# Performance work log

Hardware: AMD Instinct MI355X
Metric: run time of the kernel (lower is better)

## Reference

```python
import jax, jax.numpy as jnp
import numpy as np

BN_EPS = 1e-5


def setup_inputs() -> dict:
    key = jax.random.key(0)
    ks = jax.random.split(key, 5)
    B, T, N, C, O, K, E = 2, 4, 50000, 32, 32, 3, 800000
    x = jax.random.normal(ks[0], (B, T, N, C), dtype=jnp.float32)
    edge_index = jax.random.randint(ks[1], (2, E), 0, N, dtype=jnp.int64)
    edge_weight = jax.random.uniform(ks[2], (E,), dtype=jnp.float32)
    W = jax.random.normal(ks[3], (K, C, O), dtype=jnp.float32) * 0.05
    bias = jnp.zeros((O,), dtype=jnp.float32)
    gamma = jnp.ones((O,), dtype=jnp.float32)
    beta = jnp.zeros((O,), dtype=jnp.float32)
    return {"x": x, "edge_index": edge_index, "edge_weight": edge_weight,
            "W": W, "bias": bias, "gamma": gamma, "beta": beta}


def reference(x, edge_index, edge_weight, W, bias, gamma, beta):
    # x: [B, T, N, C]; edge_index: [2, E]; W: [K, C, O]
    B, T, N, C = x.shape
    K = W.shape[0]
    src, dst = edge_index[0], edge_index[1]

    # Scaled Laplacian L_hat = 2L/lambda_max - I with sym norm, lambda_max=2
    # => L_hat = -D^{-1/2} A D^{-1/2} (zero diagonal), PyG ChebConv default.
    deg = jax.ops.segment_sum(edge_weight, src, num_segments=N)
    safe = jnp.where(deg > 0, deg, 1.0)
    dinv = jnp.where(deg > 0, 1.0 / jnp.sqrt(safe), 0.0)
    norm = -dinv[src] * edge_weight * dinv[dst]  # [E]

    # Batch all (b, t) slices together: [N, M, C] with M = B*T
    xn = jnp.transpose(x, (2, 0, 1, 3)).reshape(N, B * T, C)

    def lap(z):  # sparse SpMM applied to every (b,t) slice at once
        return jax.ops.segment_sum(norm[:, None, None] * z[src], dst,
                                   num_segments=N)

    # Chebyshev recursion: T0 = x, T1 = L_hat x, Tk = 2 L_hat T_{k-1} - T_{k-2}
    Tx_prev2 = xn
    out = jnp.einsum('nmc,co->nmo', Tx_prev2, W[0])
    if K > 1:
        Tx_prev = lap(xn)
        out = out + jnp.einsum('nmc,co->nmo', Tx_prev, W[1])
        for k in range(2, K):
            Tx_k = 2.0 * lap(Tx_prev) - Tx_prev2
            out = out + jnp.einsum('nmc,co->nmo', Tx_k, W[k])
            Tx_prev2, Tx_prev = Tx_prev, Tx_k
    out = out + bias  # [N, M, O]

    # BatchNorm1d in training mode, applied per (b,t) slice over nodes,
    # exactly as the original per-slice loop does (biased variance).
    mean = jnp.mean(out, axis=0, keepdims=True)              # [1, M, O]
    var = jnp.mean((out - mean) ** 2, axis=0, keepdims=True)  # [1, M, O]
    y = gamma * (out - mean) * jax.lax.rsqrt(var + BN_EPS) + beta
    y = jax.nn.relu(y)

    return jnp.transpose(y.reshape(N, B, T, -1), (1, 2, 0, 3))  # [B,T,N,O]
```

## Files before the change

kernel.cpp:

```cpp
#include <hip/hip_runtime.h>

#define NNODES 50000
#define NEDGES 800000
#define MB 8
#define CF 32
#define OF 32
#define FPN 256
#define TOTAL_OUT (MB * NNODES * OF)

#define BSH 9
#define BINW 512
#define NB ((NNODES + BINW - 1) / BINW)
#define PH (NB * 2)
#define NBA 1024
#define EPB ((NEDGES + NBA - 1) / NBA)
#define CAPL 20
#define LBW 24
#define CH 8
#define BINCAP 13312
#define STCAP 7168
#define WFB ((NNODES / 16 + 3) / 4)

typedef unsigned short ushort_t;
typedef unsigned int uint_t;
typedef __attribute__((ext_vector_type(8))) short bf16x8;
typedef __attribute__((ext_vector_type(4))) float f32x4;

__device__ __forceinline__ ushort_t f2bf(float f) {
    uint_t u = __float_as_uint(f);
    u += 0x7FFFu + ((u >> 16) & 1u);
    return (ushort_t)(u >> 16);
}
__device__ __forceinline__ float bflo(uint_t u) { return __uint_as_float(u << 16); }
__device__ __forceinline__ float bfhi(uint_t u) { return __uint_as_float(u & 0xFFFF0000u); }

__device__ __forceinline__ bool detect_is64(const int* ei) {
    int lane = threadIdx.x & 63;
    int v = ei[2 * lane + 1];
    return __ballot(v != 0) == 0ULL;
}

__global__ void __launch_bounds__(256) k_build(const int* __restrict__ ei,
                                               const float* __restrict__ w,
                                               const float* __restrict__ x,
                                               int* __restrict__ g_cntD,
                                               int* __restrict__ g_cntS,
                                               int* __restrict__ g_realH,
                                               int2* __restrict__ binD,
                                               int2* __restrict__ binS,
                                               ushort_t* __restrict__ xn) {
    int blk = blockIdx.x;
    int t = threadIdx.x;
    __shared__ int l_cnt[NB];
    __shared__ int l_base[NB];
    __shared__ ushort_t l_pfx[NB + 1];
    __shared__ int l_half[PH];
    __shared__ int2 l_buf[NB][LBW];
    if (blk < NBA) {
        bool is64 = detect_is64(ei);
        const int2* ei2 = (const int2*)ei;
        for (int i = t; i < NB; i += 256) l_cnt[i] = 0;
        for (int i = t; i < PH; i += 256) l_half[i] = 0;
        __syncthreads();
        int e0 = blk * EPB;
        int e1 = min(e0 + EPB, NEDGES);
        int sreg[4];
        float wreg[4];
        #pragma unroll
        for (int i = 0; i < 4; i++) {
            int e = e0 + t + i * 256;
            bool ok = (e < e1);
            int s = 0, d = 0;
            float wt = 0.0f;
            if (ok) {
                if (is64) {
                    s = ei2[e].x;
                    d = ei2[NEDGES + e].x;
                } else {
                    s = ei[e];
                    d = ei[NEDGES + e];
                }
                wt = w[e];
            }
            sreg[i] = ok ? s : -1;
            wreg[i] = wt;
            if (ok) {
                int bin = d >> BSH;
                int half = (d >> 8) & 1;
                int2 entry;
                entry.x = s | ((d & (BINW - 1)) << 16);
                entry.y = __float_as_int(wt);
                int pos = atomicAdd(&l_cnt[bin], 1);
                if (pos < CAPL) {
                    l_buf[bin][pos] = entry;
                    atomicAdd(&l_half[bin * 2 + half], 1);
                } else {
                    int gp = atomicAdd(&g_cntD[bin], 1);
                    if (gp < BINCAP) {
                        binD[(size_t)bin * BINCAP + gp] = entry;
                        atomicAdd(&g_realH[bin * 2 + half], 1);
                    }
                }
            }
        }
        __syncthreads();
        if (t < NB) {
            int c = min(l_cnt[t], CAPL);
            int p = (c + CH - 1) & ~(CH - 1);
            for (int i = c; i < p; i++) l_buf[t][i] = make_int2(0, 0);
            l_cnt[t] = p;
            if (p > 0) l_base[t] = atomicAdd(&g_cntD[t], p);
        }
        for (int i = t; i < PH; i += 256)
            if (l_half[i] > 0) atomicAdd(&g_realH[i], l_half[i]);
        __syncthreads();
        if (t == 0) {
            int sacc = 0;
            for (int b2 = 0; b2 < NB; b2++) {
                l_pfx[b2] = (ushort_t)sacc;
                sacc += l_cnt[b2];
            }
            l_pfx[NB] = (ushort_t)sacc;
        }
        __syncthreads();
        {
            int total = l_pfx[NB];
            for (int idx = t; idx < total; idx += 256) {
                int lo = 0, hi = NB - 1;
                while (lo < hi) {
                    int mid = (lo + hi + 1) >> 1;
                    if ((int)l_pfx[mid] <= idx) lo = mid; else hi = mid - 1;
                }
                int rel = idx - (int)l_pfx[lo];
                int gp = l_base[lo] + rel;
                if (gp < BINCAP) binD[(size_t)lo * BINCAP + gp] = l_buf[lo][rel];
            }
        }
        __syncthreads();
        for (int i = t; i < NB; i += 256) l_cnt[i] = 0;
        __syncthreads();
        #pragma unroll
        for (int i = 0; i < 4; i++) {
            if (sreg[i] >= 0) {
                int s = sreg[i];
                int bin = s >> BSH;
                int2 entry;
                entry.x = s & (BINW - 1);
                entry.y = __float_as_int(wreg[i]);
                int pos = atomicAdd(&l_cnt[bin], 1);
                if (pos < CAPL) {
                    l_buf[bin][pos] = entry;
                } else {
                    int gp = atomicAdd(&g_cntS[bin], 1);
                    if (gp < BINCAP) binS[(size_t)bin * BINCAP + gp] = entry;
                }
            }
        }
        __syncthreads();
        if (t < NB) {
            int c = min(l_cnt[t], CAPL);
            int p = (c + CH - 1) & ~(CH - 1);
            for (int i = c; i < p; i++) l_buf[t][i] = make_int2(0, 0);
            l_cnt[t] = p;
            if (p > 0) l_base[t] = atomicAdd(&g_cntS[t], p);
        }
        __syncthreads();
        if (t == 0) {
            int sacc = 0;
            for (int b2 = 0; b2 < NB; b2++) {
                l_pfx[b2] = (ushort_t)sacc;
                sacc += l_cnt[b2];
            }
            l_pfx[NB] = (ushort_t)sacc;
        }
        __syncthreads();
        {
            int total = l_pfx[NB];
            for (int idx = t; idx < total; idx += 256) {
                int lo = 0, hi = NB - 1;
                while (lo < hi) {
                    int mid = (lo + hi + 1) >> 1;
                    if ((int)l_pfx[mid] <= idx) lo = mid; else hi = mid - 1;
                }
                int rel = idx - (int)l_pfx[lo];
                int gp = l_base[lo] + rel;
                if (gp < BINCAP) binS[(size_t)lo * BINCAP + gp] = l_buf[lo][rel];
            }
        }
    } else {
        int bb = blk - NBA;
        int lane = t & 63;
        int n = bb * 4 + (t >> 6);
        int m = lane >> 3;
        int c = (4 * lane) & 31;
        const float4 v = *(const float4*)(x + ((size_t)m * NNODES + n) * CF + c);
        uint2 d;
        d.x = (uint_t)f2bf(v.x) | ((uint_t)f2bf(v.y) << 16);
        d.y = (uint_t)f2bf(v.z) | ((uint_t)f2bf(v.w) << 16);
        *(uint2*)(xn + (size_t)n * FPN + 4 * lane) = d;
    }
}

__global__ void __launch_bounds__(256) k_deg(const int* __restrict__ g_cntS,
                                             const int2* __restrict__ binS,
                                             float* __restrict__ dinv) {
    __shared__ float l_acc[BINW];
    int b = blockIdx.x;
    int t = threadIdx.x;
    l_acc[t] = 0.0f;
    l_acc[t + 256] = 0.0f;
    __syncthreads();
    int cnt = min(g_cntS[b], BINCAP);
    const int2* bp = binS + (size_t)b * BINCAP;
    for (int i = t; i < cnt; i += 256) {
        int2 e = bp[i];
        atomicAdd(&l_acc[e.x], __int_as_float(e.y));
    }
    __syncthreads();
    #pragma unroll
    for (int i = 0; i < 2; i++) {
        int idx = i * 256 + t;
        int n = b * BINW + idx;
        if (n < NNODES) {
            float s = l_acc[idx];
            dinv[n] = (s > 0.0f) ? (1.0f / sqrtf(s)) : 0.0f;
        }
    }
}

__global__ void __launch_bounds__(256) k_pass2(const int* __restrict__ g_cntD,
                                               const int* __restrict__ g_realH,
                                               const int2* __restrict__ binD,
                                               const float* __restrict__ dinv,
                                               int2* __restrict__ csr,
                                               int* __restrict__ csr_off) {
    __shared__ int2 l_stage[STCAP];
    __shared__ int l_h[256];
    __shared__ int l_ws[4];
    __shared__ int l_red[4];
    __shared__ int l_tot;
    int b = blockIdx.x;
    int t = threadIdx.x;
    int bin = b >> 1, h = b & 1;
    int lane = t & 63, wv = t >> 6;

    int vb = (t < b) ? g_realH[t] : 0;
    #pragma unroll
    for (int off = 32; off >= 1; off >>= 1) vb += __shfl_down(vb, off);
    if (lane == 0) l_red[wv] = vb;
    l_h[t] = 0;
    __syncthreads();
    int base = l_red[0] + l_red[1] + l_red[2] + l_red[3];

    int cnt = min(g_cntD[bin], BINCAP);
    const int2* bp = binD + (size_t)bin * BINCAP;
    for (int i = t; i < cnt; i += 256) {
        int2 e = bp[i];
        int dl = e.x >> 16;
        if (e.y != 0 && (dl >> 8) == h) atomicAdd(&l_h[dl & 255], 1);
    }
    __syncthreads();

    int a0 = l_h[t];
    int v = a0;
    #pragma unroll
    for (int off = 1; off < 64; off <<= 1) {
        int u = __shfl_up(v, off);
        if (lane >= off) v += u;
    }
    if (lane == 63) l_ws[wv] = v;
    __syncthreads();
    int wpre = 0;
    for (int i = 0; i < wv; i++) wpre += l_ws[i];
    int excl = wpre + v - a0;

    int n = bin * BINW + h * 256 + t;
    if (n < NNODES) csr_off[n] = base + excl;
    l_h[t] = excl;
    if (t == 255) {
        l_tot = excl + a0;
        if (b == PH - 1) csr_off[NNODES] = base + excl + a0;
    }
    __syncthreads();

    for (int i = t; i < cnt; i += 256) {
        int2 e = bp[i];
        int dl = e.x >> 16;
        if (e.y != 0 && (dl >> 8) == h) {
            int src = e.x & 0xFFFF;
            int dst = bin * BINW + dl;
            float val = -dinv[src] * __int_as_float(e.y) * dinv[dst];
            int slot = atomicAdd(&l_h[dl & 255], 1);
            if (slot < STCAP) l_stage[slot] = make_int2(src, __float_as_int(val));
        }
    }
    __syncthreads();

    int tot = min(l_tot, STCAP);
    for (int i = t; i < tot; i += 256) csr[(size_t)base + i] = l_stage[i];
}

template <int PHASE>
__global__ void __launch_bounds__(256) k_spmm(const ushort_t* __restrict__ src,
                                              const ushort_t* __restrict__ xn0,
                                              const int* __restrict__ csr_off,
                                              const int2* __restrict__ csr,
                                              ushort_t* __restrict__ dst) {
    int t = threadIdx.x;
    int lane = t & 63;
    int n = __builtin_amdgcn_readfirstlane(blockIdx.x * 4 + (t >> 6));
    int off = csr_off[n];
    int cnt = min(csr_off[n + 1] - off, 64);
    float a0 = 0.0f, a1 = 0.0f, a2 = 0.0f, a3 = 0.0f;
    if (cnt > 0) {
        int j = off + min(lane, cnt - 1);
        int2 ed = csr[j];
        int cv = ed.x;
        uint_t vv = (uint_t)ed.y;
        for (int k = 0; k < cnt; k += 16) {
            int sc[16]; float v[16];
            #pragma unroll
            for (int i = 0; i < 16; i++) {
                sc[i] = __builtin_amdgcn_readlane(cv, k + i);
                float vr = __uint_as_float(__builtin_amdgcn_readlane((int)vv, k + i));
                v[i] = (k + i < cnt) ? vr : 0.0f;
            }
            uint2 u[16];
            #pragma unroll
            for (int i = 0; i < 16; i++)
                u[i] = *(const uint2*)(src + (size_t)sc[i] * FPN + 4 * lane);
            #pragma unroll
            for (int i = 0; i < 16; i++) {
                a0 += v[i] * bflo(u[i].x);
                a1 += v[i] * bfhi(u[i].x);
                a2 += v[i] * bflo(u[i].y);
                a3 += v[i] * bfhi(u[i].y);
            }
        }
    }
    if (PHASE == 2) {
        const uint2 xu = *(const uint2*)(xn0 + (size_t)n * FPN + 4 * lane);
        a0 = 2.0f * a0 - bflo(xu.x);
        a1 = 2.0f * a1 - bfhi(xu.x);
        a2 = 2.0f * a2 - bflo(xu.y);
        a3 = 2.0f * a3 - bfhi(xu.y);
    }
    uint2 d;
    d.x = (uint_t)f2bf(a0) | ((uint_t)f2bf(a1) << 16);
    d.y = (uint_t)f2bf(a2) | ((uint_t)f2bf(a3) << 16);
    *(uint2*)(dst + (size_t)n * FPN + 4 * lane) = d;
}

__global__ void k_wprep(const float* __restrict__ W, ushort_t* __restrict__ wbf) {
    int tid = threadIdx.x;
    for (int i = tid; i < 384; i += 256) {
        int k    = i >> 7;
        int rem  = i & 127;
        int oh   = rem >> 6;
        int lane = rem & 63;
        int quad = lane >> 4;
        int colc = lane & 15;
        ushort_t* d = wbf + (size_t)i * 8;
        for (int j = 0; j < 8; j++) {
            int c = quad * 8 + j;
            int o = oh * 16 + colc;
            d[j] = f2bf(W[k * (CF * OF) + c * OF + o]);
        }
    }
}

__global__ void __launch_bounds__(256) k_wfuse(const ushort_t* __restrict__ xn,
                                               const ushort_t* __restrict__ t1,
                                               const ushort_t* __restrict__ t2,
                                               const ushort_t* __restrict__ wbf,
                                               const float* __restrict__ bias,
                                               float* __restrict__ out) {
    int t = threadIdx.x;
    int lane = t & 63;
    int wv = blockIdx.x * 4 + (t >> 6);
    if (wv >= NNODES / 16) return;
    int n0 = wv * 16;
    int quad = lane >> 4, col = lane & 15;

    bf16x8 B[6];
    #pragma unroll
    for (int i = 0; i < 6; i++)
        B[i] = *(const bf16x8*)(wbf + (size_t)(i * 64 + lane) * 8);
    float blo = bias[col], bhi = bias[16 + col];

    size_t aoff = (size_t)(n0 + col) * FPN + quad * 8;
    #pragma unroll
    for (int m = 0; m < 8; m++) {
        bf16x8 A0 = *(const bf16x8*)(xn + aoff + m * 32);
        bf16x8 A1 = *(const bf16x8*)(t1 + aoff + m * 32);
        bf16x8 A2 = *(const bf16x8*)(t2 + aoff + m * 32);
        f32x4 lo = { blo, blo, blo, blo };
        f32x4 hi = { bhi, bhi, bhi, bhi };
        lo = __builtin_amdgcn_mfma_f32_16x16x32_bf16(A0, B[0], lo, 0, 0, 0);
        hi = __builtin_amdgcn_mfma_f32_16x16x32_bf16(A0, B[1], hi, 0, 0, 0);
        lo = __builtin_amdgcn_mfma_f32_16x16x32_bf16(A1, B[2], lo, 0, 0, 0);
        hi = __builtin_amdgcn_mfma_f32_16x16x32_bf16(A1, B[3], hi, 0, 0, 0);
        lo = __builtin_amdgcn_mfma_f32_16x16x32_bf16(A2, B[4], lo, 0, 0, 0);
        hi = __builtin_amdgcn_mfma_f32_16x16x32_bf16(A2, B[5], hi, 0, 0, 0);
        float* ob = out + ((size_t)m * NNODES + n0 + quad * 4) * OF + col;
        #pragma unroll
        for (int r = 0; r < 4; r++) {
            ob[(size_t)r * OF]      = lo[r];
            ob[(size_t)r * OF + 16] = hi[r];
        }
    }
}

__global__ void __launch_bounds__(256) k_stats(const float* __restrict__ out,
                                               float* __restrict__ stats) {
    int m = blockIdx.y;
    int t = threadIdx.x;
    int o4 = t & 7, row = t >> 3;
    int n0 = blockIdx.x * 1024;
    int nend = min(n0 + 1024, NNODES);
    float sx = 0, sy = 0, sz = 0, sw = 0;
    float qx = 0, qy = 0, qz = 0, qw = 0;
    for (int n = n0 + row; n < nend; n += 32) {
        const float4 v = *(const float4*)(out + ((size_t)m * NNODES + n) * OF + o4 * 4);
        sx += v.x; sy += v.y; sz += v.z; sw += v.w;
        qx += v.x * v.x; qy += v.y * v.y; qz += v.z * v.z; qw += v.w * v.w;
    }
    __shared__ float4 sS[256];
    __shared__ float4 sQ[256];
    sS[t] = make_float4(sx, sy, sz, sw);
    sQ[t] = make_float4(qx, qy, qz, qw);
    __syncthreads();
    for (int off = 16; off >= 1; off >>= 1) {
        if (row < off) {
            float4 a = sS[t], b = sS[t + off * 8];
            sS[t] = make_float4(a.x + b.x, a.y + b.y, a.z + b.z, a.w + b.w);
            float4 c = sQ[t], d = sQ[t + off * 8];
            sQ[t] = make_float4(c.x + d.x, c.y + d.y, c.z + d.z, c.w + d.w);
        }
        __syncthreads();
    }
    if (row == 0) {
        float4 s = sS[t], q = sQ[t];
        int base = m * 32 + o4 * 4;
        atomicAdd(&stats[base + 0], s.x);
        atomicAdd(&stats[base + 1], s.y);
        atomicAdd(&stats[base + 2], s.z);
        atomicAdd(&stats[base + 3], s.w);
        atomicAdd(&stats[256 + base + 0], q.x);
        atomicAdd(&stats[256 + base + 1], q.y);
        atomicAdd(&stats[256 + base + 2], q.z);
        atomicAdd(&stats[256 + base + 3], q.w);
    }
}

__global__ void __launch_bounds__(256) k_final(float* __restrict__ out,
                                               const float* __restrict__ stats,
                                               const float* __restrict__ gamma,
                                               const float* __restrict__ beta) {
    int idx4 = blockIdx.x * 256 + threadIdx.x;
    size_t base = (size_t)idx4 * 4;
    int o = (int)(base & 31);
    int m = (int)(base / ((size_t)NNODES * OF));
    int mo = m * 32 + o;
    const float4 sm = *(const float4*)(stats + mo);
    const float4 sq = *(const float4*)(stats + 256 + mo);
    const float4 g  = *(const float4*)(gamma + o);
    const float4 bt = *(const float4*)(beta + o);
    const float inv_n = 1.0f / (float)NNODES;
    float4 v = *(const float4*)(out + base);
    {
        float mean = sm.x * inv_n, var = sq.x * inv_n - mean * mean;
        float sc = g.x * rsqrtf(var + 1e-5f);
        v.x = fmaxf(v.x * sc + (bt.x - sc * mean), 0.0f);
    }
    {
        float mean = sm.y * inv_n, var = sq.y * inv_n - mean * mean;
        float sc = g.y * rsqrtf(var + 1e-5f);
        v.y = fmaxf(v.y * sc + (bt.y - sc * mean), 0.0f);
    }
    {
        float mean = sm.z * inv_n, var = sq.z * inv_n - mean * mean;
        float sc = g.z * rsqrtf(var + 1e-5f);
        v.z = fmaxf(v.z * sc + (bt.z - sc * mean), 0.0f);
    }
    {
        float mean = sm.w * inv_n, var = sq.w * inv_n - mean * mean;
        float sc = g.w * rsqrtf(var + 1e-5f);
        v.w = fmaxf(v.w * sc + (bt.w - sc * mean), 0.0f);
    }
    *(float4*)(out + base) = v;
}

extern "C" void kernel_launch(void* const* d_in, const int* in_sizes, int n_in,
                              void* d_out, int out_size, void* d_ws, size_t ws_size,
                              hipStream_t stream) {
    const float* x     = (const float*)d_in[0];
    const int*   ei    = (const int*)d_in[1];
    const float* w     = (const float*)d_in[2];
    const float* W     = (const float*)d_in[3];
    const float* bias  = (const float*)d_in[4];
    const float* gamma = (const float*)d_in[5];
    const float* beta  = (const float*)d_in[6];
    float* out = (float*)d_out;

    char* p = (char*)d_ws;
    auto alloc = [&](size_t bytes) {
        char* r = p;
        p += (bytes + 511) & ~(size_t)511;
        return r;
    };
    int*      g_cntD  = (int*)alloc((size_t)NB * 4);
    int*      g_cntS  = (int*)alloc((size_t)NB * 4);
    int*      g_realH = (int*)alloc((size_t)PH * 4);
    float*    stats   = (float*)alloc(512 * 4);
    float*    dinv    = (float*)alloc((size_t)NNODES * 4);
    int2*     binD    = (int2*)alloc((size_t)NB * BINCAP * 8);
    int2*     binS    = (int2*)alloc((size_t)NB * BINCAP * 8);
    int2*     csr     = (int2*)alloc((size_t)NEDGES * 8);
    int*      csr_off = (int*)alloc((size_t)(NNODES + 1) * 4);
    ushort_t* wbf     = (ushort_t*)alloc(384 * 8 * 2);
    ushort_t* xn      = (ushort_t*)alloc((size_t)NNODES * FPN * 2);
    ushort_t* t1      = (ushort_t*)alloc((size_t)NNODES * FPN * 2);
    ushort_t* t2      = (ushort_t*)alloc((size_t)NNODES * FPN * 2);

    size_t zlen = (char*)(stats + 512) - (char*)g_cntD;
    hipMemsetAsync(g_cntD, 0, zlen, stream);

    k_wprep<<<1, 256, 0, stream>>>(W, wbf);
    k_build<<<NBA + NNODES / 4, 256, 0, stream>>>(ei, w, x, g_cntD, g_cntS,
                                                  g_realH, binD, binS, xn);
    k_deg<<<NB, 256, 0, stream>>>(g_cntS, binS, dinv);
    k_pass2<<<PH, 256, 0, stream>>>(g_cntD, g_realH, binD, dinv, csr, csr_off);

    k_spmm<1><<<NNODES / 4, 256, 0, stream>>>(xn, xn, csr_off, csr, t1);
    k_spmm<2><<<NNODES / 4, 256, 0, stream>>>(t1, xn, csr_off, csr, t2);

    k_wfuse<<<WFB, 256, 0, stream>>>(xn, t1, t2, wbf, bias, out);

    dim3 sgrid((NNODES + 1023) / 1024, MB);
    k_stats<<<sgrid, 256, 0, stream>>>(out, stats);
    k_final<<<TOTAL_OUT / 4 / 256, 256, 0, stream>>>(out, stats, gamma, beta);
}
```

Baseline: 366.6 us.

## Fuse degree and CSR build, fold norm into SpMM, fuse second SpMM with MFMA

Merges k_deg and k_pass2 into one launch whose CSR slots sit at a fixed offset per half-bin, each row padded to a multiple of 16 with the padded count packed into csr_off. This drops the global realH prefix counts. The dinv-based normalization moves into the SpMM kernels, and the second SpMM is fused with the weight MFMA through LDS, so the t2 buffer is never written or read. The memset and weight prep fold into one init kernel. In exchange the CSR has fixed capacity with padded zero edges, per-node edges beyond 64 are silently truncated, and dinv is recomputed per edge in both SpMMs.

```diff
diff --git a/kernel.cpp b/kernel.cpp
--- a/kernel.cpp
+++ b/kernel.cpp
@@ -18,8 +18,7 @@
 #define LBW 24
 #define CH 8
 #define BINCAP 13312
-#define STCAP 7168
-#define WFB ((NNODES / 16 + 3) / 4)
+#define STCAP 7936
 
 typedef unsigned short ushort_t;
 typedef unsigned int uint_t;
@@ -38,6 +37,31 @@
     int lane = threadIdx.x & 63;
     int v = ei[2 * lane + 1];
     return __ballot(v != 0) == 0ULL;
+}
+
+__global__ void __launch_bounds__(256) k_init(const float* __restrict__ W,
+                                              ushort_t* __restrict__ wbf,
+                                              int* __restrict__ g_cntD,
+                                              int* __restrict__ g_cntS,
+                                              float* __restrict__ stats) {
+    int t = threadIdx.x;
+    if (t < NB) { g_cntD[t] = 0; g_cntS[t] = 0; }
+    stats[t] = 0.0f;
+    stats[256 + t] = 0.0f;
+    for (int i = t; i < 384; i += 256) {
+        int k    = i >> 7;
+        int rem  = i & 127;
+        int oh   = rem >> 6;
+        int lane = rem & 63;
+        int quad = lane >> 4;
+        int colc = lane & 15;
+        ushort_t* d = wbf + (size_t)i * 8;
+        for (int j = 0; j < 8; j++) {
+            int c = quad * 8 + j;
+            int o = oh * 16 + colc;
+            d[j] = f2bf(W[k * (CF * OF) + c * OF + o]);
+        }
+    }
 }
 
 __global__ void __launch_bounds__(256) k_build(const int* __restrict__ ei,
@@ -45,7 +69,6 @@
                                                const float* __restrict__ x,
                                                int* __restrict__ g_cntD,
                                                int* __restrict__ g_cntS,
-                                               int* __restrict__ g_realH,
                                                int2* __restrict__ binD,
                                                int2* __restrict__ binS,
                                                ushort_t* __restrict__ xn) {
@@ -54,13 +77,11 @@
     __shared__ int l_cnt[NB];
     __shared__ int l_base[NB];
     __shared__ ushort_t l_pfx[NB + 1];
-    __shared__ int l_half[PH];
     __shared__ int2 l_buf[NB][LBW];
     if (blk < NBA) {
         bool is64 = detect_is64(ei);
         const int2* ei2 = (const int2*)ei;
         for (int i = t; i < NB; i += 256) l_cnt[i] = 0;
-        for (int i = t; i < PH; i += 256) l_half[i] = 0;
         __syncthreads();
         int e0 = blk * EPB;
         int e1 = min(e0 + EPB, NEDGES);
@@ -86,20 +107,15 @@
             wreg[i] = wt;
             if (ok) {
                 int bin = d >> BSH;
-                int half = (d >> 8) & 1;
                 int2 entry;
                 entry.x = s | ((d & (BINW - 1)) << 16);
                 entry.y = __float_as_int(wt);
                 int pos = atomicAdd(&l_cnt[bin], 1);
                 if (pos < CAPL) {
                     l_buf[bin][pos] = entry;
-                    atomicAdd(&l_half[bin * 2 + half], 1);
                 } else {
                     int gp = atomicAdd(&g_cntD[bin], 1);
-                    if (gp < BINCAP) {
-                        binD[(size_t)bin * BINCAP + gp] = entry;
-                        atomicAdd(&g_realH[bin * 2 + half], 1);
-                    }
+                    if (gp < BINCAP) binD[(size_t)bin * BINCAP + gp] = entry;
                 }
             }
         }
@@ -111,8 +127,6 @@
             l_cnt[t] = p;
             if (p > 0) l_base[t] = atomicAdd(&g_cntD[t], p);
         }
-        for (int i = t; i < PH; i += 256)
-            if (l_half[i] > 0) atomicAdd(&g_realH[i], l_half[i]);
         __syncthreads();
         if (t == 0) {
             int sacc = 0;
@@ -201,57 +215,48 @@
     }
 }
 
-__global__ void __launch_bounds__(256) k_deg(const int* __restrict__ g_cntS,
-                                             const int2* __restrict__ binS,
-                                             float* __restrict__ dinv) {
-    __shared__ float l_acc[BINW];
+__global__ void __launch_bounds__(256) k_prep(const int* __restrict__ g_cntD,
+                                              const int* __restrict__ g_cntS,
+                                              const int2* __restrict__ binD,
+                                              const int2* __restrict__ binS,
+                                              float* __restrict__ dinv,
+                                              int2* __restrict__ csr,
+                                              int* __restrict__ csr_off) {
+    __shared__ int2 l_stage[STCAP];
+    __shared__ int l_h[256];
+    __shared__ int l_end[256];
+    __shared__ int l_ws[4];
     int b = blockIdx.x;
     int t = threadIdx.x;
-    l_acc[t] = 0.0f;
-    l_acc[t + 256] = 0.0f;
-    __syncthreads();
-    int cnt = min(g_cntS[b], BINCAP);
-    const int2* bp = binS + (size_t)b * BINCAP;
-    for (int i = t; i < cnt; i += 256) {
-        int2 e = bp[i];
-        atomicAdd(&l_acc[e.x], __int_as_float(e.y));
-    }
-    __syncthreads();
-    #pragma unroll
-    for (int i = 0; i < 2; i++) {
-        int idx = i * 256 + t;
-        int n = b * BINW + idx;
-        if (n < NNODES) {
-            float s = l_acc[idx];
-            dinv[n] = (s > 0.0f) ? (1.0f / sqrtf(s)) : 0.0f;
-        }
-    }
-}
-
-__global__ void __launch_bounds__(256) k_pass2(const int* __restrict__ g_cntD,
-                                               const int* __restrict__ g_realH,
-                                               const int2* __restrict__ binD,
-                                               const float* __restrict__ dinv,
-                                               int2* __restrict__ csr,
-                                               int* __restrict__ csr_off) {
-    __shared__ int2 l_stage[STCAP];
-    __shared__ int l_h[256];
-    __shared__ int l_ws[4];
-    __shared__ int l_red[4];
-    __shared__ int l_tot;
-    int b = blockIdx.x;
-    int t = threadIdx.x;
-    int bin = b >> 1, h = b & 1;
+    if (b < NB) {
+        float* l_acc = (float*)l_stage;
+        l_acc[t] = 0.0f;
+        l_acc[t + 256] = 0.0f;
+        __syncthreads();
+        int cnt = min(g_cntS[b], BINCAP);
+        const int2* bp = binS + (size_t)b * BINCAP;
+        for (int i = t; i < cnt; i += 256) {
+            int2 e = bp[i];
+            atomicAdd(&l_acc[e.x], __int_as_float(e.y));
+        }
+        __syncthreads();
+        #pragma unroll
+        for (int i = 0; i < 2; i++) {
+            int idx = i * 256 + t;
+            int n = b * BINW + idx;
+            if (n < NNODES) {
+                float s = l_acc[idx];
+                dinv[n] = (s > 0.0f) ? (1.0f / sqrtf(s)) : 0.0f;
+            }
+        }
+        return;
+    }
+    int b2 = b - NB;
+    int bin = b2 >> 1, h = b2 & 1;
     int lane = t & 63, wv = t >> 6;
 
-    int vb = (t < b) ? g_realH[t] : 0;
-    #pragma unroll
-    for (int off = 32; off >= 1; off >>= 1) vb += __shfl_down(vb, off);
-    if (lane == 0) l_red[wv] = vb;
     l_h[t] = 0;
     __syncthreads();
-    int base = l_red[0] + l_red[1] + l_red[2] + l_red[3];
-
     int cnt = min(g_cntD[bin], BINCAP);
     const int2* bp = binD + (size_t)bin * BINCAP;
     for (int i = t; i < cnt; i += 256) {
@@ -261,8 +266,9 @@
     }
     __syncthreads();
 
-    int a0 = l_h[t];
-    int v = a0;
+    int hreal = l_h[t];
+    int ppad = min((hreal + 15) & ~15, 64);
+    int v = ppad;
     #pragma unroll
     for (int off = 1; off < 64; off <<= 1) {
         int u = __shfl_up(v, off);
@@ -272,63 +278,62 @@
     __syncthreads();
     int wpre = 0;
     for (int i = 0; i < wv; i++) wpre += l_ws[i];
-    int excl = wpre + v - a0;
+    int excl = wpre + v - ppad;
+    int tot = l_ws[0] + l_ws[1] + l_ws[2] + l_ws[3];
+    int ztot = min(tot, STCAP);
 
     int n = bin * BINW + h * 256 + t;
-    if (n < NNODES) csr_off[n] = base + excl;
+    if (n < NNODES) csr_off[n] = ((b2 * STCAP + excl) << 3) | (ppad >> 4);
     l_h[t] = excl;
-    if (t == 255) {
-        l_tot = excl + a0;
-        if (b == PH - 1) csr_off[NNODES] = base + excl + a0;
-    }
-    __syncthreads();
-
+    l_end[t] = min(excl + ppad, STCAP);
+    __syncthreads();
+
+    for (int i = t; i < ztot; i += 256) l_stage[i] = make_int2(0, 0);
+    __syncthreads();
     for (int i = t; i < cnt; i += 256) {
         int2 e = bp[i];
         int dl = e.x >> 16;
         if (e.y != 0 && (dl >> 8) == h) {
-            int src = e.x & 0xFFFF;
-            int dst = bin * BINW + dl;
-            float val = -dinv[src] * __int_as_float(e.y) * dinv[dst];
-            int slot = atomicAdd(&l_h[dl & 255], 1);
-            if (slot < STCAP) l_stage[slot] = make_int2(src, __float_as_int(val));
-        }
-    }
-    __syncthreads();
-
-    int tot = min(l_tot, STCAP);
-    for (int i = t; i < tot; i += 256) csr[(size_t)base + i] = l_stage[i];
-}
-
-template <int PHASE>
-__global__ void __launch_bounds__(256) k_spmm(const ushort_t* __restrict__ src,
-                                              const ushort_t* __restrict__ xn0,
-                                              const int* __restrict__ csr_off,
-                                              const int2* __restrict__ csr,
-                                              ushort_t* __restrict__ dst) {
+            int node = dl & 255;
+            int slot = atomicAdd(&l_h[node], 1);
+            if (slot < l_end[node]) l_stage[slot] = make_int2(e.x & 0xFFFF, e.y);
+        }
+    }
+    __syncthreads();
+
+    for (int i = t; i < ztot; i += 256) csr[(size_t)b2 * STCAP + i] = l_stage[i];
+}
+
+__global__ void __launch_bounds__(256) k_spmm1(const ushort_t* __restrict__ xn,
+                                               const int* __restrict__ csr_off,
+                                               const int2* __restrict__ csr,
+                                               const float* __restrict__ dinv,
+                                               ushort_t* __restrict__ t1) {
     int t = threadIdx.x;
     int lane = t & 63;
     int n = __builtin_amdgcn_readfirstlane(blockIdx.x * 4 + (t >> 6));
-    int off = csr_off[n];
-    int cnt = min(csr_off[n + 1] - off, 64);
+    int pk = csr_off[n];
+    int off = pk >> 3;
+    int cnt = (pk & 7) << 4;
+    float dn = dinv[n];
     float a0 = 0.0f, a1 = 0.0f, a2 = 0.0f, a3 = 0.0f;
     if (cnt > 0) {
         int j = off + min(lane, cnt - 1);
         int2 ed = csr[j];
         int cv = ed.x;
-        uint_t vv = (uint_t)ed.y;
+        float vw = -dinv[cv] * __int_as_float(ed.y) * dn;
+        uint_t vv = __float_as_uint(vw);
         for (int k = 0; k < cnt; k += 16) {
             int sc[16]; float v[16];
             #pragma unroll
             for (int i = 0; i < 16; i++) {
                 sc[i] = __builtin_amdgcn_readlane(cv, k + i);
-                float vr = __uint_as_float(__builtin_amdgcn_readlane((int)vv, k + i));
-                v[i] = (k + i < cnt) ? vr : 0.0f;
+                v[i] = __uint_as_float(__builtin_amdgcn_readlane((int)vv, k + i));
             }
             uint2 u[16];
             #pragma unroll
             for (int i = 0; i < 16; i++)
-                u[i] = *(const uint2*)(src + (size_t)sc[i] * FPN + 4 * lane);
+                u[i] = *(const uint2*)(xn + (size_t)sc[i] * FPN + 4 * lane);
             #pragma unroll
             for (int i = 0; i < 16; i++) {
                 a0 += v[i] * bflo(u[i].x);
@@ -338,62 +343,82 @@
             }
         }
     }
-    if (PHASE == 2) {
+    uint2 d;
+    d.x = (uint_t)f2bf(a0) | ((uint_t)f2bf(a1) << 16);
+    d.y = (uint_t)f2bf(a2) | ((uint_t)f2bf(a3) << 16);
+    *(uint2*)(t1 + (size_t)n * FPN + 4 * lane) = d;
+}
+
+__global__ void __launch_bounds__(256) k_spmm2w(const ushort_t* __restrict__ t1,
+                                                const ushort_t* __restrict__ xn0,
+                                                const int* __restrict__ csr_off,
+                                                const int2* __restrict__ csr,
+                                                const float* __restrict__ dinv,
+                                                const ushort_t* __restrict__ wbf,
+                                                const float* __restrict__ bias,
+                                                float* __restrict__ out) {
+    __shared__ ushort_t lds_t2[16][264];
+    int t = threadIdx.x;
+    int lane = t & 63;
+    int wv = t >> 6;
+    int n0 = blockIdx.x * 16;
+    for (int q = 0; q < 4; q++) {
+        int n = __builtin_amdgcn_readfirstlane(n0 + wv * 4 + q);
+        int pk = csr_off[n];
+        int off = pk >> 3;
+        int cnt = (pk & 7) << 4;
+        float dn = dinv[n];
+        float a0 = 0.0f, a1 = 0.0f, a2 = 0.0f, a3 = 0.0f;
+        if (cnt > 0) {
+            int j = off + min(lane, cnt - 1);
+            int2 ed = csr[j];
+            int cv = ed.x;
+            float vw = -dinv[cv] * __int_as_float(ed.y) * dn;
+            uint_t vv = __float_as_uint(vw);
+            for (int k = 0; k < cnt; k += 16) {
+                int sc[16]; float v[16];
+                #pragma unroll
+                for (int i = 0; i < 16; i++) {
+                    sc[i] = __builtin_amdgcn_readlane(cv, k + i);
+                    v[i] = __uint_as_float(__builtin_amdgcn_readlane((int)vv, k + i));
+                }
+                uint2 u[16];
+                #pragma unroll
+                for (int i = 0; i < 16; i++)
+                    u[i] = *(const uint2*)(t1 + (size_t)sc[i] * FPN + 4 * lane);
+                #pragma unroll
+                for (int i = 0; i < 16; i++) {
+                    a0 += v[i] * bflo(u[i].x);
+                    a1 += v[i] * bfhi(u[i].x);
+                    a2 += v[i] * bflo(u[i].y);
+                    a3 += v[i] * bfhi(u[i].y);
+                }
+            }
+        }
         const uint2 xu = *(const uint2*)(xn0 + (size_t)n * FPN + 4 * lane);
         a0 = 2.0f * a0 - bflo(xu.x);
         a1 = 2.0f * a1 - bfhi(xu.x);
         a2 = 2.0f * a2 - bflo(xu.y);
         a3 = 2.0f * a3 - bfhi(xu.y);
-    }
-    uint2 d;
-    d.x = (uint_t)f2bf(a0) | ((uint_t)f2bf(a1) << 16);
-    d.y = (uint_t)f2bf(a2) | ((uint_t)f2bf(a3) << 16);
-    *(uint2*)(dst + (size_t)n * FPN + 4 * lane) = d;
-}
-
-__global__ void k_wprep(const float* __restrict__ W, ushort_t* __restrict__ wbf) {
-    int tid = threadIdx.x;
-    for (int i = tid; i < 384; i += 256) {
-        int k    = i >> 7;
-        int rem  = i & 127;
-        int oh   = rem >> 6;
-        int lane = rem & 63;
-        int quad = lane >> 4;
-        int colc = lane & 15;
-        ushort_t* d = wbf + (size_t)i * 8;
-        for (int j = 0; j < 8; j++) {
-            int c = quad * 8 + j;
-            int o = oh * 16 + colc;
-            d[j] = f2bf(W[k * (CF * OF) + c * OF + o]);
-        }
-    }
-}
-
-__global__ void __launch_bounds__(256) k_wfuse(const ushort_t* __restrict__ xn,
-                                               const ushort_t* __restrict__ t1,
-                                               const ushort_t* __restrict__ t2,
-                                               const ushort_t* __restrict__ wbf,
-                                               const float* __restrict__ bias,
-                                               float* __restrict__ out) {
-    int t = threadIdx.x;
-    int lane = t & 63;
-    int wv = blockIdx.x * 4 + (t >> 6);
-    if (wv >= NNODES / 16) return;
-    int n0 = wv * 16;
+        uint2 d;
+        d.x = (uint_t)f2bf(a0) | ((uint_t)f2bf(a1) << 16);
+        d.y = (uint_t)f2bf(a2) | ((uint_t)f2bf(a3) << 16);
+        *(uint2*)&lds_t2[wv * 4 + q][4 * lane] = d;
+    }
+    __syncthreads();
     int quad = lane >> 4, col = lane & 15;
-
     bf16x8 B[6];
     #pragma unroll
     for (int i = 0; i < 6; i++)
         B[i] = *(const bf16x8*)(wbf + (size_t)(i * 64 + lane) * 8);
     float blo = bias[col], bhi = bias[16 + col];
-
     size_t aoff = (size_t)(n0 + col) * FPN + quad * 8;
     #pragma unroll
-    for (int m = 0; m < 8; m++) {
-        bf16x8 A0 = *(const bf16x8*)(xn + aoff + m * 32);
+    for (int mi = 0; mi < 2; mi++) {
+        int m = wv * 2 + mi;
+        bf16x8 A0 = *(const bf16x8*)(xn0 + aoff + m * 32);
         bf16x8 A1 = *(const bf16x8*)(t1 + aoff + m * 32);
-        bf16x8 A2 = *(const bf16x8*)(t2 + aoff + m * 32);
+        bf16x8 A2 = *(const bf16x8*)&lds_t2[col][quad * 8 + m * 32];
         f32x4 lo = { blo, blo, blo, blo };
         f32x4 hi = { bhi, bhi, bhi, bhi };
         lo = __builtin_amdgcn_mfma_f32_16x16x32_bf16(A0, B[0], lo, 0, 0, 0);
@@ -511,32 +536,24 @@
     };
     int*      g_cntD  = (int*)alloc((size_t)NB * 4);
     int*      g_cntS  = (int*)alloc((size_t)NB * 4);
-    int*      g_realH = (int*)alloc((size_t)PH * 4);
     float*    stats   = (float*)alloc(512 * 4);
     float*    dinv    = (float*)alloc((size_t)NNODES * 4);
     int2*     binD    = (int2*)alloc((size_t)NB * BINCAP * 8);
     int2*     binS    = (int2*)alloc((size_t)NB * BINCAP * 8);
-    int2*     csr     = (int2*)alloc((size_t)NEDGES * 8);
+    int2*     csr     = (int2*)alloc((size_t)PH * STCAP * 8);
     int*      csr_off = (int*)alloc((size_t)(NNODES + 1) * 4);
     ushort_t* wbf     = (ushort_t*)alloc(384 * 8 * 2);
     ushort_t* xn      = (ushort_t*)alloc((size_t)NNODES * FPN * 2);
     ushort_t* t1      = (ushort_t*)alloc((size_t)NNODES * FPN * 2);
-    ushort_t* t2      = (ushort_t*)alloc((size_t)NNODES * FPN * 2);
-
-    size_t zlen = (char*)(stats + 512) - (char*)g_cntD;
-    hipMemsetAsync(g_cntD, 0, zlen, stream);
-
-    k_wprep<<<1, 256, 0, stream>>>(W, wbf);
+
+    k_init<<<1, 256, 0, stream>>>(W, wbf, g_cntD, g_cntS, stats);
     k_build<<<NBA + NNODES / 4, 256, 0, stream>>>(ei, w, x, g_cntD, g_cntS,
-                                                  g_realH, binD, binS, xn);
-    k_deg<<<NB, 256, 0, stream>>>(g_cntS, binS, dinv);
-    k_pass2<<<PH, 256, 0, stream>>>(g_cntD, g_realH, binD, dinv, csr, csr_off);
-
-    k_spmm<1><<<NNODES / 4, 256, 0, stream>>>(xn, xn, csr_off, csr, t1);
-    k_spmm<2><<<NNODES / 4, 256, 0, stream>>>(t1, xn, csr_off, csr, t2);
-
-    k_wfuse<<<WFB, 256, 0, stream>>>(xn, t1, t2, wbf, bias, out);
-
+                                                  binD, binS, xn);
+    k_prep<<<NB + PH, 256, 0, stream>>>(g_cntD, g_cntS, binD, binS,
+                                        dinv, csr, csr_off);
+    k_spmm1<<<NNODES / 4, 256, 0, stream>>>(xn, csr_off, csr, dinv, t1);
+    k_spmm2w<<<NNODES / 16, 256, 0, stream>>>(t1, xn, csr_off, csr, dinv,
+                                              wbf, bias, out);
     dim3 sgrid((NNODES + 1023) / 1024, MB);
     k_stats<<<sgrid, 256, 0, stream>>>(out, stats);
     k_final<<<TOTAL_OUT / 4 / 256, 256, 0, stream>>>(out, stats, gamma, beta);
```

Result: faster. 334.0 us (-8.9%).
